# Performance work log

Hardware: AMD Instinct MI355X
Metric: run time of the kernel (lower is better)

## Reference

```python
import jax, jax.numpy as jnp
import numpy as np
from jax import lax

T, B, H, NF, FS = 512, 128, 512, 128, 5  # max_seq_len, batch, hidden, num_filters, filter_size


def setup_inputs() -> dict:
    key = jax.random.key(0)
    ks = jax.random.split(key, 16)
    inp = {
        "encoder_output": jax.random.normal(ks[0], (T, B, H), dtype=jnp.float32),
        "lengths": jax.random.randint(ks[1], (B,), 1, T + 1, dtype=jnp.int64 if jax.config.jax_enable_x64 else jnp.int32),
    }
    for w in range(1, FS + 1):
        inp[f"conv_w{w}"] = jax.random.normal(ks[1 + w], (NF, 1, H, w), dtype=jnp.float32) * 0.02
        inp[f"conv_b{w}"] = jnp.zeros((NF,), dtype=jnp.float32)
    inp["fc1_w"] = jax.random.normal(ks[12], (100, FS * NF), dtype=jnp.float32) * 0.05
    inp["fc1_b"] = jnp.zeros((100,), dtype=jnp.float32)
    inp["fc2_w"] = jax.random.normal(ks[13], (1, 100), dtype=jnp.float32) * 0.1
    inp["fc2_b"] = jnp.zeros((1,), dtype=jnp.float32)
    return inp


def _raw_reshape(x, L):
    # Faithful to torch .contiguous().view(1,1,H,-1) on a [L,H] slice:
    # row-major flatten of first L rows, reshaped to [H, L], zero-padded to [H, T].
    flat = x.reshape(-1)                       # [T*H]
    h = jnp.arange(H)[:, None]                 # [H,1]
    l = jnp.arange(T)[None, :]                 # [1,T]
    return jnp.where(l < L, flat[h * L + l], 0.0)  # [H,T]


def reference(encoder_output, lengths,
              conv_w1, conv_b1, conv_w2, conv_b2, conv_w3, conv_b3,
              conv_w4, conv_b4, conv_w5, conv_b5,
              fc1_w, fc1_b, fc2_w, fc2_b):
    # encoder_output: [T, B, H]; per-sample raw reshape to [H, T] (length-dependent)
    X = jax.vmap(_raw_reshape, in_axes=(1, 0))(encoder_output, lengths)  # [B,H,T]
    X4 = X[:, None, :, :]                                               # [B,1,H,T]
    Leff = jnp.maximum(lengths, FS)  # torch code zero-pads width to >= filter_size
    conv_ws = [conv_w1, conv_w2, conv_w3, conv_w4, conv_w5]
    conv_bs = [conv_b1, conv_b2, conv_b3, conv_b4, conv_b5]
    pools = []
    for w in range(1, FS + 1):
        out = lax.conv_general_dilated(
            X4, conv_ws[w - 1], window_strides=(1, 1), padding='VALID',
            dimension_numbers=('NCHW', 'OIHW', 'NCHW'))          # [B,NF,1,T-w+1]
        r = jax.nn.relu(out[:, :, 0, :] + conv_bs[w - 1][None, :, None])  # [B,NF,Tw]
        tpos = jnp.arange(T - w + 1)
        valid = tpos[None, :] < (Leff - w + 1)[:, None]          # [B,Tw]
        r = jnp.where(valid[:, None, :], r, 0.0)                 # relu>=0, so 0 is safe for max
        pools.append(r.max(axis=2))                              # [B,NF]
    feat = jnp.concatenate(pools, axis=1)                        # [B,FS*NF]
    fc1 = feat @ fc1_w.T + fc1_b
    fc2 = fc1 @ fc2_w.T + fc2_b
    probs = jax.nn.sigmoid(fc2)                                  # [B,1]
    return probs[:, None, :]                                     # [B,1,1] == torch.stack of [1,1]
```

## Files before the change

kernel.cpp:

```cpp
#include <hip/hip_runtime.h>
#include <hip/hip_bf16.h>

#define TT 512
#define BB 128
#define HH 512
#define NFC 128

typedef short v8s __attribute__((ext_vector_type(8)));
typedef float v4f __attribute__((ext_vector_type(4)));

__device__ __forceinline__ unsigned short f2bf(float x) {
    unsigned u = __float_as_uint(x);
    unsigned r = (u + 0x7fffu + ((u >> 16) & 1u)) >> 16;
    return (unsigned short)r;
}

__global__ void prep_all(const float* __restrict__ enc, const int* __restrict__ lengths,
                         unsigned short* __restrict__ Xg,
                         const float* __restrict__ w1, const float* __restrict__ w2,
                         const float* __restrict__ w3, const float* __restrict__ w4,
                         const float* __restrict__ w5, unsigned short* __restrict__ Wg,
                         float* __restrict__ pools,
                         const float* __restrict__ fc1w, const float* __restrict__ fc1b,
                         const float* __restrict__ fc2w, const float* __restrict__ fc2b,
                         float* __restrict__ v, int* __restrict__ wl) {
    int blk = blockIdx.x;
    int tid = threadIdx.x;
    if (blk < 8192) {
        __shared__ float tile[64 * 65];
        int b = blk >> 6;
        int lc = (blk >> 3) & 7;
        int hc = blk & 7;
        int L = lengths[b];
        int Leff = L > 5 ? L : 5;
        int l0 = lc * 64, h0 = hc * 64;
        if (l0 >= Leff + 127) return;
        int lx = tid & 63;
        int hq = tid >> 6;
        #pragma unroll
        for (int r = 0; r < 16; ++r) {
            int hl = hq * 16 + r;
            int l = l0 + lx;
            float val = 0.f;
            if (l < L) {
                int i = (h0 + hl) * L + l;
                val = enc[(i >> 9) * (BB * HH) + b * HH + (i & 511)];
            }
            tile[hl * 65 + lx] = val;
        }
        __syncthreads();
        int hg = tid & 15;
        #pragma unroll
        for (int r = 0; r < 4; ++r) {
            int lloc = (tid >> 4) + r * 16;
            int n = b * 512 + l0 + lloc;
            ushort4 pk;
            pk.x = f2bf(tile[(hg * 4 + 0) * 65 + lloc]);
            pk.y = f2bf(tile[(hg * 4 + 1) * 65 + lloc]);
            pk.z = f2bf(tile[(hg * 4 + 2) * 65 + lloc]);
            pk.w = f2bf(tile[(hg * 4 + 3) * 65 + lloc]);
            *(ushort4*)&Xg[n * 512 + h0 + hg * 4] = pk;
        }
    } else if (blk < 12288) {
        int o = (blk - 8192) * 256 + tid;
        int j   = o & 7;
        int ln  = (o >> 3) & 63;
        int mi  = (o >> 9) & 3;
        int kt  = (o >> 11) & 15;
        int wmm = (o >> 15) & 1;
        int mtt = o >> 16;
        int row = mtt * 128 + wmm * 64 + mi * 16 + (ln & 15);
        int k   = kt * 32 + (ln >> 4) * 8 + j;
        int f = row >> 4, sl = row & 15;
        float val = 0.f;
        if (sl < 15) {
            int w, jj;
            if (sl < 1)       { w = 1; jj = sl; }
            else if (sl < 3)  { w = 2; jj = sl - 1; }
            else if (sl < 6)  { w = 3; jj = sl - 3; }
            else if (sl < 10) { w = 4; jj = sl - 6; }
            else              { w = 5; jj = sl - 10; }
            const float* wp = (w == 1) ? w1 : (w == 2) ? w2 : (w == 3) ? w3 : (w == 4) ? w4 : w5;
            val = wp[f * (HH * w) + k * w + jj];
        }
        Wg[o] = f2bf(val);
    } else if (blk < 12608) {
        int i = (blk - 12288) * 256 + tid;
        if (i < BB * 5 * NFC) pools[i] = 0.f;
    } else if (blk == 12608) {
        for (int k = tid; k < 640; k += 256) {
            float s = 0.f;
            for (int o = 0; o < 100; ++o) s += fc2w[o] * fc1w[o * 640 + k];
            v[k] = s;
        }
        if (tid == 0) {
            float c = fc2b[0];
            for (int o = 0; o < 100; ++o) c += fc2w[o] * fc1b[o];
            v[640] = c;
        }
    } else {
        __shared__ int cnt;
        if (tid == 0) cnt = 0;
        __syncthreads();
        for (int it = tid; it < 640; it += 256) {
            int b = it / 5, tt = it % 5;
            int L = lengths[b];
            int Leff = L > 5 ? L : 5;
            int n0 = tt * 124 - ((tt >> 2) * 112);
            if (n0 < Leff) {
                int pos = atomicAdd(&cnt, 1);
                wl[pos] = (b << 3) | tt;
            }
        }
        __syncthreads();
        if (tid == 0) wl[640] = cnt;
    }
}

#define GLDS(GP, LP) __builtin_amdgcn_global_load_lds(                            \
    (const __attribute__((address_space(1))) unsigned int*)(GP),                  \
    (__attribute__((address_space(3))) unsigned int*)(LP), 16, 0, 0)

#define LOADA4(B0, B1, B2, B3, PTR) do {                                          \
    asm volatile("global_load_dwordx4 %0, %1, off"             : "=v"(B0) : "v"(PTR) : "memory"); \
    asm volatile("global_load_dwordx4 %0, %1, off offset:1024" : "=v"(B1) : "v"(PTR) : "memory"); \
    asm volatile("global_load_dwordx4 %0, %1, off offset:2048" : "=v"(B2) : "v"(PTR) : "memory"); \
    asm volatile("global_load_dwordx4 %0, %1, off offset:3072" : "=v"(B3) : "v"(PTR) : "memory"); \
} while (0)

#define MFMA16(A0, A1, A2, A3) do {                                               \
    acc[0][0] = __builtin_amdgcn_mfma_f32_16x16x32_bf16(A0, Bf0, acc[0][0], 0, 0, 0); \
    acc[0][1] = __builtin_amdgcn_mfma_f32_16x16x32_bf16(A0, Bf1, acc[0][1], 0, 0, 0); \
    acc[0][2] = __builtin_amdgcn_mfma_f32_16x16x32_bf16(A0, Bf2, acc[0][2], 0, 0, 0); \
    acc[0][3] = __builtin_amdgcn_mfma_f32_16x16x32_bf16(A0, Bf3, acc[0][3], 0, 0, 0); \
    acc[1][0] = __builtin_amdgcn_mfma_f32_16x16x32_bf16(A1, Bf0, acc[1][0], 0, 0, 0); \
    acc[1][1] = __builtin_amdgcn_mfma_f32_16x16x32_bf16(A1, Bf1, acc[1][1], 0, 0, 0); \
    acc[1][2] = __builtin_amdgcn_mfma_f32_16x16x32_bf16(A1, Bf2, acc[1][2], 0, 0, 0); \
    acc[1][3] = __builtin_amdgcn_mfma_f32_16x16x32_bf16(A1, Bf3, acc[1][3], 0, 0, 0); \
    acc[2][0] = __builtin_amdgcn_mfma_f32_16x16x32_bf16(A2, Bf0, acc[2][0], 0, 0, 0); \
    acc[2][1] = __builtin_amdgcn_mfma_f32_16x16x32_bf16(A2, Bf1, acc[2][1], 0, 0, 0); \
    acc[2][2] = __builtin_amdgcn_mfma_f32_16x16x32_bf16(A2, Bf2, acc[2][2], 0, 0, 0); \
    acc[2][3] = __builtin_amdgcn_mfma_f32_16x16x32_bf16(A2, Bf3, acc[2][3], 0, 0, 0); \
    acc[3][0] = __builtin_amdgcn_mfma_f32_16x16x32_bf16(A3, Bf0, acc[3][0], 0, 0, 0); \
    acc[3][1] = __builtin_amdgcn_mfma_f32_16x16x32_bf16(A3, Bf1, acc[3][1], 0, 0, 0); \
    acc[3][2] = __builtin_amdgcn_mfma_f32_16x16x32_bf16(A3, Bf2, acc[3][2], 0, 0, 0); \
    acc[3][3] = __builtin_amdgcn_mfma_f32_16x16x32_bf16(A3, Bf3, acc[3][3], 0, 0, 0); \
} while (0)

#define BREAD(SLOT)                                                               \
    v8s Bf0 = *(const v8s*)&ldsB[(SLOT) * 4096 + (wn * 64 +  0 + llo) * 32 + psw * 8]; \
    v8s Bf1 = *(const v8s*)&ldsB[(SLOT) * 4096 + (wn * 64 + 16 + llo) * 32 + psw * 8]; \
    v8s Bf2 = *(const v8s*)&ldsB[(SLOT) * 4096 + (wn * 64 + 32 + llo) * 32 + psw * 8]; \
    v8s Bf3 = *(const v8s*)&ldsB[(SLOT) * 4096 + (wn * 64 + 48 + llo) * 32 + psw * 8];

__global__ __launch_bounds__(256, 4)
void conv_gemm(const unsigned short* __restrict__ Wg, const unsigned short* __restrict__ Xg,
               const int* __restrict__ lengths, const int* __restrict__ wl,
               const float* __restrict__ cb1, const float* __restrict__ cb2,
               const float* __restrict__ cb3, const float* __restrict__ cb4,
               const float* __restrict__ cb5,
               float* __restrict__ pools) {
    __shared__ __align__(16) char smem[33024];
    unsigned short* ldsB = (unsigned short*)smem;
    float* Gs = (float*)smem;

    int cnt = wl[640];
    int g = blockIdx.x;
    int xcd = g & 7;
    int q = g >> 3;
    int mt = q & 15;
    int wk = (q >> 4) * 8 + xcd;
    if (wk >= cnt) return;
    int item = wl[wk];
    int b = item >> 3, tt = item & 7;
    int n0 = tt * 124 - ((tt >> 2) * 112);
    int L = lengths[b];
    int Leff = L > 5 ? L : 5;

    int tid = threadIdx.x;
    int wid = tid >> 6, lane = tid & 63;
    int wm = wid >> 1, wn = wid & 1;
    int llo = lane & 15, quad = lane >> 4;
    int psw = quad ^ ((llo >> 1) & 3);

    int nb0 = b * 512 + n0;

    v4f acc[4][4];
    #pragma unroll
    for (int i = 0; i < 4; ++i)
        #pragma unroll
        for (int j = 0; j < 4; ++j) acc[i][j] = v4f{0.f, 0.f, 0.f, 0.f};

    int srow = lane >> 2;
    int gchunk = (lane & 3) ^ ((lane >> 3) & 3);
    const unsigned short* gB = Xg + (nb0 + wid * 32 + srow) * 512 + gchunk * 8;
    int sdst = (wid * 32) * 32;

    const unsigned short* pA = Wg + (mt * 2 + wm) * 32768 + lane * 8;

    GLDS(gB,                 &ldsB[0 * 4096 + sdst]);
    GLDS(gB + 16 * 512,      &ldsB[0 * 4096 + sdst + 512]);
    GLDS(gB + 32,            &ldsB[1 * 4096 + sdst]);
    GLDS(gB + 16 * 512 + 32, &ldsB[1 * 4096 + sdst + 512]);
    v8s AfA0, AfA1, AfA2, AfA3;
    v8s AfB0, AfB1, AfB2, AfB3;
    LOADA4(AfA0, AfA1, AfA2, AfA3, pA);
    {
        const unsigned short* pA1 = pA + 2048;
        LOADA4(AfB0, AfB1, AfB2, AfB3, pA1);
    }
    const unsigned short* pAc = pA + 4096;

    #pragma unroll 1
    for (int i = 0; i < 7; ++i) {
        int sb = (i & 1) * 2;
        int tb = 2 - sb;
        asm volatile("s_waitcnt vmcnt(8)" ::: "memory");
        __builtin_amdgcn_s_barrier();
        {
            const unsigned short* gs = gB + (2 * i + 2) * 32;
            GLDS(gs,                 &ldsB[tb * 4096 + sdst]);
            GLDS(gs + 16 * 512,      &ldsB[tb * 4096 + sdst + 512]);
            GLDS(gs + 32,            &ldsB[(tb + 1) * 4096 + sdst]);
            GLDS(gs + 16 * 512 + 32, &ldsB[(tb + 1) * 4096 + sdst + 512]);
        }
        {
            BREAD(sb);
            asm volatile("s_waitcnt vmcnt(8)" ::: "memory");
            __builtin_amdgcn_sched_barrier(0);
            __builtin_amdgcn_s_setprio(1);
            MFMA16(AfA0, AfA1, AfA2, AfA3);
            __builtin_amdgcn_s_setprio(0);
            LOADA4(AfA0, AfA1, AfA2, AfA3, pAc);
            pAc += 2048;
        }
        {
            BREAD(sb + 1);
            asm volatile("s_waitcnt vmcnt(8)" ::: "memory");
            __builtin_amdgcn_sched_barrier(0);
            __builtin_amdgcn_s_setprio(1);
            MFMA16(AfB0, AfB1, AfB2, AfB3);
            __builtin_amdgcn_s_setprio(0);
            LOADA4(AfB0, AfB1, AfB2, AfB3, pAc);
            pAc += 2048;
        }
    }
    asm volatile("s_waitcnt vmcnt(8)" ::: "memory");
    __builtin_amdgcn_s_barrier();
    {
        BREAD(2);
        asm volatile("s_waitcnt vmcnt(4)" ::: "memory");
        __builtin_amdgcn_sched_barrier(0);
        __builtin_amdgcn_s_setprio(1);
        MFMA16(AfA0, AfA1, AfA2, AfA3);
        __builtin_amdgcn_s_setprio(0);
    }
    {
        BREAD(3);
        asm volatile("s_waitcnt vmcnt(0)" ::: "memory");
        __builtin_amdgcn_sched_barrier(0);
        __builtin_amdgcn_s_setprio(1);
        MFMA16(AfB0, AfB1, AfB2, AfB3);
        __builtin_amdgcn_s_setprio(0);
    }

    __syncthreads();

    #pragma unroll
    for (int phase = 0; phase < 2; ++phase) {
        if (wm == phase) {
            #pragma unroll
            for (int mi = 0; mi < 4; ++mi)
                #pragma unroll
                for (int ni = 0; ni < 4; ++ni)
                    #pragma unroll
                    for (int r = 0; r < 4; ++r)
                        Gs[(mi * 16 + quad * 4 + r) * 129 + wn * 64 + ni * 16 + llo] = acc[mi][ni][r];
        }
        __syncthreads();
        {
            int fl = wid;
            int f = mt * 8 + phase * 4 + fl;
            float bias[5] = {cb1[f], cb2[f], cb3[f], cb4[f], cb5[f]};
            const int basew[5] = {0, 1, 3, 6, 10};
            const float* gbase = &Gs[(fl * 16) * 129 + lane];
            float vm[5];
            #pragma unroll
            for (int w = 1; w <= 5; ++w) {
                float s0 = 0.f, s1 = 0.f;
                #pragma unroll
                for (int j = 0; j < w; ++j) {
                    int o = basew[w - 1] * 129 + j * 130;
                    s0 += gbase[o];
                    s1 += gbase[o + 64];
                }
                int limv = Leff - w + 1 - n0;
                int lim = 128 - w; if (limv - 1 < lim) lim = limv - 1;
                float m = -1.f;
                if (lane <= lim)      m = fmaxf(m, fmaxf(s0 + bias[w - 1], 0.f));
                if (lane + 64 <= lim) m = fmaxf(m, fmaxf(s1 + bias[w - 1], 0.f));
                vm[w - 1] = m;
            }
            #pragma unroll
            for (int off = 32; off >= 1; off >>= 1) {
                #pragma unroll
                for (int w = 0; w < 5; ++w)
                    vm[w] = fmaxf(vm[w], __shfl_xor(vm[w], off));
            }
            if (lane == 0 && vm[0] >= 0.f) atomicMax((int*)&pools[(b * 5 + 0) * NFC + f], __float_as_int(vm[0]));
            if (lane == 1 && vm[1] >= 0.f) atomicMax((int*)&pools[(b * 5 + 1) * NFC + f], __float_as_int(vm[1]));
            if (lane == 2 && vm[2] >= 0.f) atomicMax((int*)&pools[(b * 5 + 2) * NFC + f], __float_as_int(vm[2]));
            if (lane == 3 && vm[3] >= 0.f) atomicMax((int*)&pools[(b * 5 + 3) * NFC + f], __float_as_int(vm[3]));
            if (lane == 4 && vm[4] >= 0.f) atomicMax((int*)&pools[(b * 5 + 4) * NFC + f], __float_as_int(vm[4]));
        }
        __syncthreads();
    }
}

__global__ void head(const float* __restrict__ pools, const float* __restrict__ v,
                     float* __restrict__ out) {
    int b = blockIdx.x;
    int tid = threadIdx.x;
    float s = 0.f;
    for (int k = tid; k < 640; k += 256) s += pools[b * 640 + k] * v[k];
    __shared__ float red[256];
    red[tid] = s;
    __syncthreads();
    for (int st = 128; st; st >>= 1) {
        if (tid < st) red[tid] += red[tid + st];
        __syncthreads();
    }
    if (tid == 0) out[b] = 1.f / (1.f + expf(-(red[0] + v[640])));
}

extern "C" void kernel_launch(void* const* d_in, const int* in_sizes, int n_in,
                              void* d_out, int out_size, void* d_ws, size_t ws_size,
                              hipStream_t stream) {
    const float* enc  = (const float*)d_in[0];
    const int* lens   = (const int*)d_in[1];
    const float* w1   = (const float*)d_in[2];
    const float* b1   = (const float*)d_in[3];
    const float* w2   = (const float*)d_in[4];
    const float* b2   = (const float*)d_in[5];
    const float* w3   = (const float*)d_in[6];
    const float* b3   = (const float*)d_in[7];
    const float* w4   = (const float*)d_in[8];
    const float* b4   = (const float*)d_in[9];
    const float* w5   = (const float*)d_in[10];
    const float* b5   = (const float*)d_in[11];
    const float* fc1w = (const float*)d_in[12];
    const float* fc1b = (const float*)d_in[13];
    const float* fc2w = (const float*)d_in[14];
    const float* fc2b = (const float*)d_in[15];
    float* out = (float*)d_out;

    unsigned short* Xg = (unsigned short*)d_ws;
    unsigned short* Wg = Xg + 33554432;
    float* pools  = (float*)(Wg + 1048576);
    float* vbuf   = pools + 81920;
    int* wlist    = (int*)(vbuf + 641);

    prep_all<<<12610, 256, 0, stream>>>(enc, lens, Xg, w1, w2, w3, w4, w5, Wg, pools,
                                        fc1w, fc1b, fc2w, fc2b, vbuf, wlist);
    conv_gemm<<<10240, 256, 0, stream>>>(Wg, Xg, lens, wlist, b1, b2, b3, b4, b5, pools);
    head<<<128, 256, 0, stream>>>(pools, vbuf, out);
}
```

Before: 344.3 us.

## Switch conv GEMM from 16x16x32 to 32x32x16 bf16 MFMA tiles

Replaces the sixteen 16x16x32 MFMAs per k-step with eight 32x32x16 MFMAs covering the same 64x64 warp tile. The weight pre-pack layout, the LDS B-fragment addressing and the accumulator-to-LDS epilogue are all remapped to match the 32x32 operand and output layout. The main loop is also fully unrolled. The aim is fewer MFMA issues and fewer LDS fragment reads per k-step, at the cost of longer-latency instructions and a changed swizzle that could cause LDS bank conflicts or break correctness if the mapping is off.

```diff
diff --git a/kernel.cpp b/kernel.cpp
--- a/kernel.cpp
+++ b/kernel.cpp
@@ -8,6 +8,7 @@
 
 typedef short v8s __attribute__((ext_vector_type(8)));
 typedef float v4f __attribute__((ext_vector_type(4)));
+typedef float v16f __attribute__((ext_vector_type(16)));
 
 __device__ __forceinline__ unsigned short f2bf(float x) {
     unsigned u = __float_as_uint(x);
@@ -65,12 +66,13 @@
         int o = (blk - 8192) * 256 + tid;
         int j   = o & 7;
         int ln  = (o >> 3) & 63;
-        int mi  = (o >> 9) & 3;
+        int s   = (o >> 9) & 1;
+        int mi2 = (o >> 10) & 1;
         int kt  = (o >> 11) & 15;
         int wmm = (o >> 15) & 1;
         int mtt = o >> 16;
-        int row = mtt * 128 + wmm * 64 + mi * 16 + (ln & 15);
-        int k   = kt * 32 + (ln >> 4) * 8 + j;
+        int row = mtt * 128 + wmm * 64 + mi2 * 32 + (ln & 31);
+        int k   = kt * 32 + s * 16 + (ln >> 5) * 8 + j;
         int f = row >> 4, sl = row & 15;
         float val = 0.f;
         if (sl < 15) {
@@ -128,30 +130,22 @@
     asm volatile("global_load_dwordx4 %0, %1, off offset:3072" : "=v"(B3) : "v"(PTR) : "memory"); \
 } while (0)
 
-#define MFMA16(A0, A1, A2, A3) do {                                               \
-    acc[0][0] = __builtin_amdgcn_mfma_f32_16x16x32_bf16(A0, Bf0, acc[0][0], 0, 0, 0); \
-    acc[0][1] = __builtin_amdgcn_mfma_f32_16x16x32_bf16(A0, Bf1, acc[0][1], 0, 0, 0); \
-    acc[0][2] = __builtin_amdgcn_mfma_f32_16x16x32_bf16(A0, Bf2, acc[0][2], 0, 0, 0); \
-    acc[0][3] = __builtin_amdgcn_mfma_f32_16x16x32_bf16(A0, Bf3, acc[0][3], 0, 0, 0); \
-    acc[1][0] = __builtin_amdgcn_mfma_f32_16x16x32_bf16(A1, Bf0, acc[1][0], 0, 0, 0); \
-    acc[1][1] = __builtin_amdgcn_mfma_f32_16x16x32_bf16(A1, Bf1, acc[1][1], 0, 0, 0); \
-    acc[1][2] = __builtin_amdgcn_mfma_f32_16x16x32_bf16(A1, Bf2, acc[1][2], 0, 0, 0); \
-    acc[1][3] = __builtin_amdgcn_mfma_f32_16x16x32_bf16(A1, Bf3, acc[1][3], 0, 0, 0); \
-    acc[2][0] = __builtin_amdgcn_mfma_f32_16x16x32_bf16(A2, Bf0, acc[2][0], 0, 0, 0); \
-    acc[2][1] = __builtin_amdgcn_mfma_f32_16x16x32_bf16(A2, Bf1, acc[2][1], 0, 0, 0); \
-    acc[2][2] = __builtin_amdgcn_mfma_f32_16x16x32_bf16(A2, Bf2, acc[2][2], 0, 0, 0); \
-    acc[2][3] = __builtin_amdgcn_mfma_f32_16x16x32_bf16(A2, Bf3, acc[2][3], 0, 0, 0); \
-    acc[3][0] = __builtin_amdgcn_mfma_f32_16x16x32_bf16(A3, Bf0, acc[3][0], 0, 0, 0); \
-    acc[3][1] = __builtin_amdgcn_mfma_f32_16x16x32_bf16(A3, Bf1, acc[3][1], 0, 0, 0); \
-    acc[3][2] = __builtin_amdgcn_mfma_f32_16x16x32_bf16(A3, Bf2, acc[3][2], 0, 0, 0); \
-    acc[3][3] = __builtin_amdgcn_mfma_f32_16x16x32_bf16(A3, Bf3, acc[3][3], 0, 0, 0); \
+#define MFMA8(A0, A1, A2, A3) do {                                                \
+    acc00 = __builtin_amdgcn_mfma_f32_32x32x16_bf16(A0, Bf00, acc00, 0, 0, 0);    \
+    acc01 = __builtin_amdgcn_mfma_f32_32x32x16_bf16(A0, Bf10, acc01, 0, 0, 0);    \
+    acc10 = __builtin_amdgcn_mfma_f32_32x32x16_bf16(A2, Bf00, acc10, 0, 0, 0);    \
+    acc11 = __builtin_amdgcn_mfma_f32_32x32x16_bf16(A2, Bf10, acc11, 0, 0, 0);    \
+    acc00 = __builtin_amdgcn_mfma_f32_32x32x16_bf16(A1, Bf01, acc00, 0, 0, 0);    \
+    acc01 = __builtin_amdgcn_mfma_f32_32x32x16_bf16(A1, Bf11, acc01, 0, 0, 0);    \
+    acc10 = __builtin_amdgcn_mfma_f32_32x32x16_bf16(A3, Bf01, acc10, 0, 0, 0);    \
+    acc11 = __builtin_amdgcn_mfma_f32_32x32x16_bf16(A3, Bf11, acc11, 0, 0, 0);    \
 } while (0)
 
-#define BREAD(SLOT)                                                               \
-    v8s Bf0 = *(const v8s*)&ldsB[(SLOT) * 4096 + (wn * 64 +  0 + llo) * 32 + psw * 8]; \
-    v8s Bf1 = *(const v8s*)&ldsB[(SLOT) * 4096 + (wn * 64 + 16 + llo) * 32 + psw * 8]; \
-    v8s Bf2 = *(const v8s*)&ldsB[(SLOT) * 4096 + (wn * 64 + 32 + llo) * 32 + psw * 8]; \
-    v8s Bf3 = *(const v8s*)&ldsB[(SLOT) * 4096 + (wn * 64 + 48 + llo) * 32 + psw * 8];
+#define BREAD32(SLOT)                                                             \
+    v8s Bf00 = *(const v8s*)&ldsB[(SLOT) * 4096 + bb0];                           \
+    v8s Bf01 = *(const v8s*)&ldsB[(SLOT) * 4096 + bb1];                           \
+    v8s Bf10 = *(const v8s*)&ldsB[(SLOT) * 4096 + bb0 + 1024];                    \
+    v8s Bf11 = *(const v8s*)&ldsB[(SLOT) * 4096 + bb1 + 1024];
 
 __global__ __launch_bounds__(256, 4)
 void conv_gemm(const unsigned short* __restrict__ Wg, const unsigned short* __restrict__ Xg,
@@ -181,20 +175,20 @@
     int wid = tid >> 6, lane = tid & 63;
     int wm = wid >> 1, wn = wid & 1;
     int llo = lane & 15, quad = lane >> 4;
-    int psw = quad ^ ((llo >> 1) & 3);
+    int l31 = lane & 31, hi = lane >> 5;
+    int xorv = (lane >> 1) & 3;
 
     int nb0 = b * 512 + n0;
 
-    v4f acc[4][4];
-    #pragma unroll
-    for (int i = 0; i < 4; ++i)
-        #pragma unroll
-        for (int j = 0; j < 4; ++j) acc[i][j] = v4f{0.f, 0.f, 0.f, 0.f};
+    v16f acc00 = {}, acc01 = {}, acc10 = {}, acc11 = {};
 
     int srow = lane >> 2;
     int gchunk = (lane & 3) ^ ((lane >> 3) & 3);
     const unsigned short* gB = Xg + (nb0 + wid * 32 + srow) * 512 + gchunk * 8;
     int sdst = (wid * 32) * 32;
+
+    int bb0 = (wn * 64 + l31) * 32 + ((hi) ^ xorv) * 8;
+    int bb1 = (wn * 64 + l31) * 32 + ((2 + hi) ^ xorv) * 8;
 
     const unsigned short* pA = Wg + (mt * 2 + wm) * 32768 + lane * 8;
 
@@ -211,10 +205,10 @@
     }
     const unsigned short* pAc = pA + 4096;
 
-    #pragma unroll 1
+    #pragma unroll
     for (int i = 0; i < 7; ++i) {
-        int sb = (i & 1) * 2;
-        int tb = 2 - sb;
+        const int sb = (i & 1) * 2;
+        const int tb = 2 - sb;
         asm volatile("s_waitcnt vmcnt(8)" ::: "memory");
         __builtin_amdgcn_s_barrier();
         {
@@ -225,21 +219,21 @@
             GLDS(gs + 16 * 512 + 32, &ldsB[(tb + 1) * 4096 + sdst + 512]);
         }
         {
-            BREAD(sb);
+            BREAD32(sb);
             asm volatile("s_waitcnt vmcnt(8)" ::: "memory");
             __builtin_amdgcn_sched_barrier(0);
             __builtin_amdgcn_s_setprio(1);
-            MFMA16(AfA0, AfA1, AfA2, AfA3);
+            MFMA8(AfA0, AfA1, AfA2, AfA3);
             __builtin_amdgcn_s_setprio(0);
             LOADA4(AfA0, AfA1, AfA2, AfA3, pAc);
             pAc += 2048;
         }
         {
-            BREAD(sb + 1);
+            BREAD32(sb + 1);
             asm volatile("s_waitcnt vmcnt(8)" ::: "memory");
             __builtin_amdgcn_sched_barrier(0);
             __builtin_amdgcn_s_setprio(1);
-            MFMA16(AfB0, AfB1, AfB2, AfB3);
+            MFMA8(AfB0, AfB1, AfB2, AfB3);
             __builtin_amdgcn_s_setprio(0);
             LOADA4(AfB0, AfB1, AfB2, AfB3, pAc);
             pAc += 2048;
@@ -248,19 +242,19 @@
     asm volatile("s_waitcnt vmcnt(8)" ::: "memory");
     __builtin_amdgcn_s_barrier();
     {
-        BREAD(2);
+        BREAD32(2);
         asm volatile("s_waitcnt vmcnt(4)" ::: "memory");
         __builtin_amdgcn_sched_barrier(0);
         __builtin_amdgcn_s_setprio(1);
-        MFMA16(AfA0, AfA1, AfA2, AfA3);
+        MFMA8(AfA0, AfA1, AfA2, AfA3);
         __builtin_amdgcn_s_setprio(0);
     }
     {
-        BREAD(3);
+        BREAD32(3);
         asm volatile("s_waitcnt vmcnt(0)" ::: "memory");
         __builtin_amdgcn_sched_barrier(0);
         __builtin_amdgcn_s_setprio(1);
-        MFMA16(AfB0, AfB1, AfB2, AfB3);
+        MFMA8(AfB0, AfB1, AfB2, AfB3);
         __builtin_amdgcn_s_setprio(0);
     }
 
@@ -270,12 +264,13 @@
     for (int phase = 0; phase < 2; ++phase) {
         if (wm == phase) {
             #pragma unroll
-            for (int mi = 0; mi < 4; ++mi)
-                #pragma unroll
-                for (int ni = 0; ni < 4; ++ni)
-                    #pragma unroll
-                    for (int r = 0; r < 4; ++r)
-                        Gs[(mi * 16 + quad * 4 + r) * 129 + wn * 64 + ni * 16 + llo] = acc[mi][ni][r];
+            for (int r = 0; r < 16; ++r) {
+                int row = (r & 3) + 8 * (r >> 2) + 4 * hi;
+                Gs[(row)      * 129 + wn * 64 +  0 + l31] = acc00[r];
+                Gs[(row)      * 129 + wn * 64 + 32 + l31] = acc01[r];
+                Gs[(row + 32) * 129 + wn * 64 +  0 + l31] = acc10[r];
+                Gs[(row + 32) * 129 + wn * 64 + 32 + l31] = acc11[r];
+            }
         }
         __syncthreads();
         {
```

Result: slower. 355.0 us (+3.1%).
